# Kernel tuning notes

Measured on AMD Instinct MI355X. Metric: run time of the kernel, lower is better.

## Reference

```python
import jax, jax.numpy as jnp
import numpy as np

DIM = 128
NUM_HEADS = 4
WIN = 16  # effective window: window_size(8) * sqrt(dim_t=4)
N = WIN * WIN
B_ = 512
NW = 64


def _relative_position_index(wh, ww):
    coords = np.stack(np.meshgrid(np.arange(wh), np.arange(ww), indexing='ij'))  # (2,wh,ww)
    cf = coords.reshape(2, -1)
    rel = cf[:, :, None] - cf[:, None, :]  # (2,N,N)
    rel = rel.transpose(1, 2, 0).copy()
    rel[:, :, 0] += wh - 1
    rel[:, :, 1] += ww - 1
    rel[:, :, 0] *= 2 * ww - 1
    return rel.sum(-1).astype(np.int32)  # (N,N)


def setup_inputs() -> dict:
    key = jax.random.key(0)
    ks = jax.random.split(key, 7)
    inputs = jax.random.normal(ks[0], (B_, N, DIM), dtype=jnp.float32)
    mask = jax.random.normal(ks[1], (NW, N, N), dtype=jnp.float32)
    qkv_w = jax.random.normal(ks[2], (3 * DIM, DIM), dtype=jnp.float32) * 0.02
    qkv_b = jnp.zeros((3 * DIM,), dtype=jnp.float32)
    proj_w = jax.random.normal(ks[3], (DIM, DIM), dtype=jnp.float32) * 0.02
    proj_b = jnp.zeros((DIM,), dtype=jnp.float32)
    table_sz = (2 * WIN - 1) * (2 * WIN - 1)  # 961
    bias_table = jax.random.normal(ks[4], (table_sz, NUM_HEADS), dtype=jnp.float32) * 0.02
    rel_idx = jnp.asarray(_relative_position_index(WIN, WIN))  # (N,N) int32
    return {"inputs": inputs, "mask": mask, "qkv_w": qkv_w, "qkv_b": qkv_b,
            "proj_w": proj_w, "proj_b": proj_b, "bias_table": bias_table,
            "rel_idx": rel_idx}


def reference(inputs, mask, qkv_w, qkv_b, proj_w, proj_b, bias_table, rel_idx):
    B, Nn, C = inputs.shape
    H = bias_table.shape[1]
    Dh = C // H
    scale = Dh ** -0.5
    qkv = (inputs @ qkv_w.T + qkv_b).reshape(B, Nn, 3, H, Dh)
    qkv = jnp.transpose(qkv, (2, 0, 3, 1, 4))  # (3,B,H,N,Dh)
    q, k, v = qkv[0] * scale, qkv[1], qkv[2]
    attn = jnp.einsum('bhnd,bhmd->bhnm', q, k)  # (B,H,N,N)
    rpb = jnp.transpose(bias_table[rel_idx], (2, 0, 1))  # (H,N,N)
    attn = attn + rpb[None]
    nW = mask.shape[0]
    attn = attn.reshape(B // nW, nW, H, Nn, Nn) + mask[None, :, None]
    attn = jax.nn.softmax(attn.reshape(B, H, Nn, Nn), axis=-1)
    out = jnp.einsum('bhnm,bhmd->bhnd', attn, v)
    out = jnp.transpose(out, (0, 2, 1, 3)).reshape(B, Nn, C)
    return out @ proj_w.T + proj_b
```

## Files before the change

### kernel.cpp

```cpp
#include <hip/hip_runtime.h>

typedef __bf16 bf16;
typedef __bf16 bf16x8 __attribute__((ext_vector_type(8)));
typedef __bf16 bf16x4 __attribute__((ext_vector_type(4)));
typedef float f32x4 __attribute__((ext_vector_type(4)));

static __device__ __forceinline__ f32x4 mfma16(bf16x8 a, bf16x8 b, f32x4 c) {
  return __builtin_amdgcn_mfma_f32_16x16x32_bf16(a, b, c, 0, 0, 0);
}

static __device__ __forceinline__ bf16x8 pk8(f32x4 a, f32x4 b) {
  bf16x8 r;
  r[0] = (bf16)a[0]; r[1] = (bf16)a[1]; r[2] = (bf16)a[2]; r[3] = (bf16)a[3];
  r[4] = (bf16)b[0]; r[5] = (bf16)b[1]; r[6] = (bf16)b[2]; r[7] = (bf16)b[3];
  return r;
}

__global__ void k0_rpb(const float* __restrict__ bt, const int* __restrict__ ri,
                       float* __restrict__ rpb) {
  int t = blockIdx.x * 256 + threadIdx.x;
  int idx = ri[t];
  f32x4 v = *(const f32x4*)(bt + idx * 4);
#pragma unroll
  for (int h = 0; h < 4; ++h) rpb[h * 65536 + t] = v[h];
}

__global__ void k0_w(const float* __restrict__ qw, const float* __restrict__ pw,
                     bf16* __restrict__ wqb, bf16* __restrict__ wpb) {
  int t = blockIdx.x * 256 + threadIdx.x;
  if (t < 49152) wqb[t] = (bf16)qw[t];
  else wpb[t - 49152] = (bf16)pw[t - 49152];
}

__global__ void __launch_bounds__(256, 3)
k1_qkv(const float* __restrict__ x, const bf16* __restrict__ wqb,
       const float* __restrict__ qb, bf16* __restrict__ q_s,
       bf16* __restrict__ k_s, bf16* __restrict__ vt) {
  __shared__ bf16 xsm[16384];
  const int tid = threadIdx.x;
  const int wv = tid >> 6, ln = tid & 15, qd = (tid >> 4) & 3;
  const int b = blockIdx.x >> 1, half = blockIdx.x & 1;
  const int rg = wv >> 1, cg = wv & 1;

#pragma unroll
  for (int j = 0; j < 8; ++j) {
    const int bidx = j * 256 + tid;
    const int row = bidx >> 4, c = bidx & 15;
    const float* g = x + (size_t)(b * 256 + half * 128 + row) * 128 + c * 8;
    f32x4 a = *(const f32x4*)g, b2 = *(const f32x4*)(g + 4);
    *(bf16x8*)(xsm + row * 128 + ((c ^ (row & 7)) * 8)) = pk8(a, b2);
  }
  __syncthreads();

  f32x4 acc[4][4];
  bf16x8 xfk[4];

#pragma unroll
  for (int ch = 0; ch < 2; ++ch) {
#pragma unroll
    for (int mt = 0; mt < 4; ++mt)
#pragma unroll
      for (int nt = 0; nt < 4; ++nt) acc[mt][nt] = (f32x4){0.f, 0.f, 0.f, 0.f};
#pragma unroll
    for (int ks = 0; ks < 4; ++ks) {
#pragma unroll
      for (int nt = 0; nt < 4; ++nt) {
        const int row_l = rg * 64 + nt * 16 + ln;
        xfk[nt] = *(const bf16x8*)(xsm + row_l * 128 + (((ks * 4 + qd) ^ (ln & 7)) * 8));
      }
#pragma unroll
      for (int mt = 0; mt < 4; ++mt) {
        bf16x8 wf = *(const bf16x8*)(wqb + (size_t)(ch * 128 + cg * 64 + mt * 16 + ln) * 128 +
                                     ks * 32 + qd * 8);
#pragma unroll
        for (int nt = 0; nt < 4; ++nt) acc[mt][nt] = mfma16(wf, xfk[nt], acc[mt][nt]);
      }
    }
    const float scl = ch ? 1.0f : 0.17677669529663689f;
#pragma unroll
    for (int mt = 0; mt < 4; ++mt) {
      const int c0 = cg * 64 + mt * 16 + qd * 4;
      f32x4 b4 = *(const f32x4*)(qb + ch * 128 + c0);
      const int hh = c0 >> 5, d0 = c0 & 31;
#pragma unroll
      for (int nt = 0; nt < 4; ++nt) {
        const int nr = half * 128 + rg * 64 + nt * 16 + ln;
        bf16x4 o;
#pragma unroll
        for (int r = 0; r < 4; ++r) o[r] = (bf16)((acc[mt][nt][r] + b4[r]) * scl);
        const size_t base = (size_t)(b * 4 + hh) * 8192;
        if (ch == 0) {
          *(bf16x4*)(q_s + base + nr * 32 + d0) = o;
        } else {
          const int cb = (d0 >> 3) ^ (nr & 3) ^ ((nr >> 2) & 3);
          *(bf16x4*)(k_s + base + nr * 32 + cb * 8 + (d0 & 7)) = o;
        }
      }
    }
  }

#pragma unroll
  for (int nt = 0; nt < 4; ++nt)
#pragma unroll
    for (int mt = 0; mt < 4; ++mt) acc[nt][mt] = (f32x4){0.f, 0.f, 0.f, 0.f};
#pragma unroll
  for (int ks = 0; ks < 4; ++ks) {
#pragma unroll
    for (int nt = 0; nt < 4; ++nt) {
      const int row_l = rg * 64 + nt * 16 + ln;
      xfk[nt] = *(const bf16x8*)(xsm + row_l * 128 + (((ks * 4 + qd) ^ (ln & 7)) * 8));
    }
#pragma unroll
    for (int mt = 0; mt < 4; ++mt) {
      bf16x8 wf = *(const bf16x8*)(wqb + (size_t)(256 + cg * 64 + mt * 16 + ln) * 128 +
                                   ks * 32 + qd * 8);
#pragma unroll
      for (int nt = 0; nt < 4; ++nt) acc[nt][mt] = mfma16(xfk[nt], wf, acc[nt][mt]);
    }
  }
#pragma unroll
  for (int nt = 0; nt < 4; ++nt)
#pragma unroll
    for (int mt = 0; mt < 4; ++mt) {
      const int c = cg * 64 + mt * 16 + ln;
      const float bb = qb[256 + c];
      const int hh = c >> 5, dd = c & 31;
      const int n0 = half * 128 + rg * 64 + nt * 16 + qd * 4;
      bf16x4 o;
#pragma unroll
      for (int r = 0; r < 4; ++r) o[r] = (bf16)(acc[nt][mt][r] + bb);
      const int p = (n0 >> 3) ^ (dd & 7);
      *(bf16x4*)(vt + (size_t)(b * 4 + hh) * 8192 + dd * 256 + p * 8 + (n0 & 7)) = o;
    }
}

__global__ void __launch_bounds__(256, 3)
k2_attn(const bf16* __restrict__ q_s, const bf16* __restrict__ k_s,
        const bf16* __restrict__ vt, const float* __restrict__ mask,
        const float* __restrict__ rpb, float* __restrict__ ao) {
  __shared__ bf16 ksm[8192];
  __shared__ bf16 vsm[8192];
  __shared__ bf16 psm[8192];
  const int tid = threadIdx.x, wv = tid >> 6;
  const int ln = tid & 15, qd = (tid >> 4) & 3;
  const int w = blockIdx.x & 63, h = (blockIdx.x >> 6) & 3, rh = blockIdx.x >> 8;
  const int s = rh * 4 + wv;
  const int swzk = qd ^ (ln & 3) ^ ((ln >> 2) & 3);

  bf16x4 cmb[16];
  {
    const int n = s * 16 + ln;
#pragma unroll
    for (int mt = 0; mt < 16; ++mt) {
      f32x4 m4 = *(const f32x4*)(mask + ((size_t)w * 256 + n) * 256 + mt * 16 + qd * 4);
      f32x4 r4 = *(const f32x4*)(rpb + (size_t)h * 65536 + n * 256 + mt * 16 + qd * 4);
      bf16x4 cv;
#pragma unroll
      for (int r = 0; r < 4; ++r) cv[r] = (bf16)(m4[r] + r4[r]);
      cmb[mt] = cv;
    }
  }

  bf16x8 kr[4], vr[4];
  {
    const size_t base = (size_t)(w * 4 + h) * 8192;
#pragma unroll
    for (int i = 0; i < 4; ++i) {
      kr[i] = *(const bf16x8*)(k_s + base + i * 2048 + tid * 8);
      vr[i] = *(const bf16x8*)(vt + base + i * 2048 + tid * 8);
    }
  }

  for (int ib = 0; ib < 8; ++ib) {
    const int b = w + ib * 64;
    __syncthreads();
#pragma unroll
    for (int i = 0; i < 4; ++i) {
      *(bf16x8*)(ksm + i * 2048 + tid * 8) = kr[i];
      *(bf16x8*)(vsm + i * 2048 + tid * 8) = vr[i];
    }
    __syncthreads();
    if (ib < 7) {
      const size_t base = (size_t)((w + (ib + 1) * 64) * 4 + h) * 8192;
#pragma unroll
      for (int i = 0; i < 4; ++i) {
        kr[i] = *(const bf16x8*)(k_s + base + i * 2048 + tid * 8);
        vr[i] = *(const bf16x8*)(vt + base + i * 2048 + tid * 8);
      }
    }

    bf16x8 qf = *(const bf16x8*)(q_s + (size_t)(b * 4 + h) * 8192 + (s * 16 + ln) * 32 + qd * 8);
    float sum = 0.f;
    f32x4 accO[2];
    accO[0] = (f32x4){0.f, 0.f, 0.f, 0.f};
    accO[1] = (f32x4){0.f, 0.f, 0.f, 0.f};
    bf16* pb = psm + wv * 2048 + ln * 128;

#pragma unroll
    for (int hk = 0; hk < 2; ++hk) {
      f32x4 acc[8];
#pragma unroll
      for (int i = 0; i < 8; ++i) acc[i] = (f32x4){0.f, 0.f, 0.f, 0.f};
#pragma unroll
      for (int i = 0; i < 8; ++i) {
        const int m = (hk * 8 + i) * 16 + ln;
        bf16x8 af = *(const bf16x8*)(ksm + m * 32 + swzk * 8);
        acc[i] = mfma16(af, qf, acc[i]);
      }
#pragma unroll
      for (int i = 0; i < 8; ++i) {
        const int mt = hk * 8 + i;
        bf16x4 pv;
#pragma unroll
        for (int r = 0; r < 4; ++r) {
          float p = __expf(acc[i][r] + (float)cmb[mt][r]);
          sum += p;
          pv[r] = (bf16)p;
        }
        const int p16 = (i * 2 + (qd >> 1)) ^ (ln & 7);
        *(bf16x4*)(pb + p16 * 8 + (qd & 1) * 4) = pv;
      }
#pragma unroll
      for (int kt = 0; kt < 4; ++kt) {
        bf16x8 pf = *(const bf16x8*)(pb + (((kt * 4 + qd) ^ (ln & 7)) * 8));
#pragma unroll
        for (int ct = 0; ct < 2; ++ct) {
          const int d = ct * 16 + ln;
          const int p32 = ((hk * 4 + kt) * 4 + qd) ^ (d & 7);
          bf16x8 vf = *(const bf16x8*)(vsm + d * 256 + p32 * 8);
          accO[ct] = mfma16(pf, vf, accO[ct]);
        }
      }
    }
    sum += __shfl_xor(sum, 16);
    sum += __shfl_xor(sum, 32);
    const float linv = 1.0f / sum;
#pragma unroll
    for (int r = 0; r < 4; ++r) {
      const float lb = __shfl(linv, qd * 4 + r);
      const size_t orow = (size_t)(b * 256 + s * 16 + qd * 4 + r) * 128 + h * 32;
#pragma unroll
      for (int ct = 0; ct < 2; ++ct) ao[orow + ct * 16 + ln] = accO[ct][r] * lb;
    }
  }
}

__global__ void __launch_bounds__(256, 3)
k3_proj(const float* __restrict__ xin, const bf16* __restrict__ wpb,
        const float* __restrict__ pbias, float* __restrict__ out) {
  __shared__ bf16 xsm[16384];
  const int tid = threadIdx.x;
  const int wv = tid >> 6, ln = tid & 15, qd = (tid >> 4) & 3;
  const int rg = wv >> 1, cg = wv & 1;
  const size_t row0 = (size_t)blockIdx.x * 128;

#pragma unroll
  for (int j = 0; j < 8; ++j) {
    const int bidx = j * 256 + tid;
    const int row = bidx >> 4, c = bidx & 15;
    const float* g = xin + (row0 + row) * 128 + c * 8;
    f32x4 a = *(const f32x4*)g, b2 = *(const f32x4*)(g + 4);
    *(bf16x8*)(xsm + row * 128 + ((c ^ (row & 7)) * 8)) = pk8(a, b2);
  }
  __syncthreads();

  f32x4 acc[4][4];
  bf16x8 xfk[4];
#pragma unroll
  for (int mt = 0; mt < 4; ++mt)
#pragma unroll
    for (int nt = 0; nt < 4; ++nt) acc[mt][nt] = (f32x4){0.f, 0.f, 0.f, 0.f};
#pragma unroll
  for (int ks = 0; ks < 4; ++ks) {
#pragma unroll
    for (int nt = 0; nt < 4; ++nt) {
      const int row_l = rg * 64 + nt * 16 + ln;
      xfk[nt] = *(const bf16x8*)(xsm + row_l * 128 + (((ks * 4 + qd) ^ (ln & 7)) * 8));
    }
#pragma unroll
    for (int mt = 0; mt < 4; ++mt) {
      bf16x8 wf = *(const bf16x8*)(wpb + (size_t)(cg * 64 + mt * 16 + ln) * 128 +
                                   ks * 32 + qd * 8);
#pragma unroll
      for (int nt = 0; nt < 4; ++nt) acc[mt][nt] = mfma16(wf, xfk[nt], acc[mt][nt]);
    }
  }
#pragma unroll
  for (int mt = 0; mt < 4; ++mt) {
    const int c0 = cg * 64 + mt * 16 + qd * 4;
    f32x4 b4 = *(const f32x4*)(pbias + c0);
#pragma unroll
    for (int nt = 0; nt < 4; ++nt) {
      f32x4 o;
#pragma unroll
      for (int r = 0; r < 4; ++r) o[r] = acc[mt][nt][r] + b4[r];
      *(f32x4*)(out + (row0 + rg * 64 + nt * 16 + ln) * 128 + c0) = o;
    }
  }
}

extern "C" void kernel_launch(void* const* d_in, const int* in_sizes, int n_in,
                              void* d_out, int out_size, void* d_ws, size_t ws_size,
                              hipStream_t stream) {
  const float* x = (const float*)d_in[0];
  const float* mask = (const float*)d_in[1];
  const float* qkv_w = (const float*)d_in[2];
  const float* qkv_b = (const float*)d_in[3];
  const float* proj_w = (const float*)d_in[4];
  const float* proj_b = (const float*)d_in[5];
  const float* bias_table = (const float*)d_in[6];
  const int* rel_idx = (const int*)d_in[7];

  char* ws = (char*)d_ws;
  bf16* q_s = (bf16*)ws;
  bf16* k_s = (bf16*)(ws + 33554432ll);
  bf16* vt = (bf16*)(ws + 67108864ll);
  float* rpb = (float*)(ws + 100663296ll);
  bf16* wqb = (bf16*)(ws + 101711872ll);
  bf16* wpb = wqb + 49152;
  float* ao = (float*)d_out;

  k0_rpb<<<dim3(256), dim3(256), 0, stream>>>(bias_table, rel_idx, rpb);
  k0_w<<<dim3(256), dim3(256), 0, stream>>>(qkv_w, proj_w, wqb, wpb);
  k1_qkv<<<dim3(1024), dim3(256), 0, stream>>>(x, wqb, qkv_b, q_s, k_s, vt);
  k2_attn<<<dim3(1024), dim3(256), 0, stream>>>(q_s, k_s, vt, mask, rpb, ao);
  k3_proj<<<dim3(1024), dim3(256), 0, stream>>>(ao, wpb, proj_b, (float*)d_out);
}
```

Measured before the change: 311.5 us.

## Restructure attention to one wave per head, keep K/V in registers

```diff
diff --git a/kernel.cpp b/kernel.cpp
--- a/kernel.cpp
+++ b/kernel.cpp
@@ -16,20 +16,28 @@
   return r;
 }
 
-__global__ void k0_rpb(const float* __restrict__ bt, const int* __restrict__ ri,
-                       float* __restrict__ rpb) {
-  int t = blockIdx.x * 256 + threadIdx.x;
-  int idx = ri[t];
-  f32x4 v = *(const f32x4*)(bt + idx * 4);
-#pragma unroll
-  for (int h = 0; h < 4; ++h) rpb[h * 65536 + t] = v[h];
-}
-
-__global__ void k0_w(const float* __restrict__ qw, const float* __restrict__ pw,
-                     bf16* __restrict__ wqb, bf16* __restrict__ wpb) {
-  int t = blockIdx.x * 256 + threadIdx.x;
-  if (t < 49152) wqb[t] = (bf16)qw[t];
-  else wpb[t - 49152] = (bf16)pw[t - 49152];
+__global__ void k0_prep(const float* __restrict__ qw, const float* __restrict__ pw,
+                        const float* __restrict__ bt, const int* __restrict__ ri,
+                        const float* __restrict__ mask, bf16* __restrict__ wqb,
+                        bf16* __restrict__ wpb, bf16* __restrict__ rpb_bf,
+                        bf16* __restrict__ mask_bf) {
+  const int bid = blockIdx.x, tid = threadIdx.x;
+  if (bid < 256) {
+    int t = bid * 256 + tid;
+    if (t < 49152) wqb[t] = (bf16)qw[t];
+    else wpb[t - 49152] = (bf16)pw[t - 49152];
+  } else if (bid < 512) {
+    int t = (bid - 256) * 256 + tid;
+    int idx = ri[t];
+    f32x4 v = *(const f32x4*)(bt + idx * 4);
+#pragma unroll
+    for (int h = 0; h < 4; ++h) rpb_bf[h * 65536 + t] = (bf16)v[h];
+  } else {
+    int i = (bid - 512) * 256 + tid;
+    f32x4 a = *(const f32x4*)(mask + (size_t)i * 8);
+    f32x4 b = *(const f32x4*)(mask + (size_t)i * 8 + 4);
+    *(bf16x8*)(mask_bf + (size_t)i * 8) = pk8(a, b);
+  }
 }
 
 __global__ void __launch_bounds__(256, 3)
@@ -77,6 +85,7 @@
       }
     }
     const float scl = ch ? 1.0f : 0.17677669529663689f;
+    bf16* dst = ch ? k_s : q_s;
 #pragma unroll
     for (int mt = 0; mt < 4; ++mt) {
       const int c0 = cg * 64 + mt * 16 + qd * 4;
@@ -88,13 +97,7 @@
         bf16x4 o;
 #pragma unroll
         for (int r = 0; r < 4; ++r) o[r] = (bf16)((acc[mt][nt][r] + b4[r]) * scl);
-        const size_t base = (size_t)(b * 4 + hh) * 8192;
-        if (ch == 0) {
-          *(bf16x4*)(q_s + base + nr * 32 + d0) = o;
-        } else {
-          const int cb = (d0 >> 3) ^ (nr & 3) ^ ((nr >> 2) & 3);
-          *(bf16x4*)(k_s + base + nr * 32 + cb * 8 + (d0 & 7)) = o;
-        }
+        *(bf16x4*)(dst + (size_t)(b * 4 + hh) * 8192 + nr * 32 + d0) = o;
       }
     }
   }
@@ -129,91 +132,63 @@
       bf16x4 o;
 #pragma unroll
       for (int r = 0; r < 4; ++r) o[r] = (bf16)(acc[nt][mt][r] + bb);
-      const int p = (n0 >> 3) ^ (dd & 7);
-      *(bf16x4*)(vt + (size_t)(b * 4 + hh) * 8192 + dd * 256 + p * 8 + (n0 & 7)) = o;
-    }
-}
-
-__global__ void __launch_bounds__(256, 3)
+      *(bf16x4*)(vt + (size_t)(b * 4 + hh) * 8192 + dd * 256 + n0) = o;
+    }
+}
+
+__global__ void __launch_bounds__(64, 2)
 k2_attn(const bf16* __restrict__ q_s, const bf16* __restrict__ k_s,
-        const bf16* __restrict__ vt, const float* __restrict__ mask,
-        const float* __restrict__ rpb, float* __restrict__ ao) {
-  __shared__ bf16 ksm[8192];
-  __shared__ bf16 vsm[8192];
-  __shared__ bf16 psm[8192];
-  const int tid = threadIdx.x, wv = tid >> 6;
-  const int ln = tid & 15, qd = (tid >> 4) & 3;
-  const int w = blockIdx.x & 63, h = (blockIdx.x >> 6) & 3, rh = blockIdx.x >> 8;
-  const int s = rh * 4 + wv;
-  const int swzk = qd ^ (ln & 3) ^ ((ln >> 2) & 3);
-
-  bf16x4 cmb[16];
-  {
-    const int n = s * 16 + ln;
-#pragma unroll
-    for (int mt = 0; mt < 16; ++mt) {
-      f32x4 m4 = *(const f32x4*)(mask + ((size_t)w * 256 + n) * 256 + mt * 16 + qd * 4);
-      f32x4 r4 = *(const f32x4*)(rpb + (size_t)h * 65536 + n * 256 + mt * 16 + qd * 4);
-      bf16x4 cv;
-#pragma unroll
-      for (int r = 0; r < 4; ++r) cv[r] = (bf16)(m4[r] + r4[r]);
-      cmb[mt] = cv;
-    }
-  }
-
-  bf16x8 kr[4], vr[4];
-  {
-    const size_t base = (size_t)(w * 4 + h) * 8192;
-#pragma unroll
-    for (int i = 0; i < 4; ++i) {
-      kr[i] = *(const bf16x8*)(k_s + base + i * 2048 + tid * 8);
-      vr[i] = *(const bf16x8*)(vt + base + i * 2048 + tid * 8);
-    }
-  }
-
-  for (int ib = 0; ib < 8; ++ib) {
-    const int b = w + ib * 64;
-    __syncthreads();
-#pragma unroll
-    for (int i = 0; i < 4; ++i) {
-      *(bf16x8*)(ksm + i * 2048 + tid * 8) = kr[i];
-      *(bf16x8*)(vsm + i * 2048 + tid * 8) = vr[i];
-    }
-    __syncthreads();
-    if (ib < 7) {
-      const size_t base = (size_t)((w + (ib + 1) * 64) * 4 + h) * 8192;
-#pragma unroll
-      for (int i = 0; i < 4; ++i) {
-        kr[i] = *(const bf16x8*)(k_s + base + i * 2048 + tid * 8);
-        vr[i] = *(const bf16x8*)(vt + base + i * 2048 + tid * 8);
-      }
-    }
-
-    bf16x8 qf = *(const bf16x8*)(q_s + (size_t)(b * 4 + h) * 8192 + (s * 16 + ln) * 32 + qd * 8);
+        const bf16* __restrict__ vt, const bf16* __restrict__ mask_bf,
+        const bf16* __restrict__ rpb_bf, float* __restrict__ ao) {
+  __shared__ bf16 psm[2048];
+  const int tid = threadIdx.x, ln = tid & 15, qd = tid >> 4;
+  const int h = blockIdx.x & 3, b = blockIdx.x >> 2, w = b & 63;
+
+  const size_t panel = (size_t)(b * 4 + h) * 8192;
+  bf16x8 kf[16], vf[16];
+#pragma unroll
+  for (int mt = 0; mt < 16; ++mt)
+    kf[mt] = *(const bf16x8*)(k_s + panel + (mt * 16 + ln) * 32 + qd * 8);
+#pragma unroll
+  for (int k8 = 0; k8 < 8; ++k8)
+#pragma unroll
+    for (int ct = 0; ct < 2; ++ct)
+      vf[k8 * 2 + ct] = *(const bf16x8*)(vt + panel + (ct * 16 + ln) * 256 + k8 * 32 + qd * 8);
+
+  const bf16* mrow = mask_bf + (size_t)w * 65536;
+  const bf16* rrow = rpb_bf + (size_t)h * 65536;
+  const bf16* qp = q_s + panel;
+  bf16* pb = psm + ln * 128;
+
+  for (int s = 0; s < 16; ++s) {
+    bf16x8 qf = *(const bf16x8*)(qp + (s * 16 + ln) * 32 + qd * 8);
+    const int nrow = s * 16 + ln;
     float sum = 0.f;
     f32x4 accO[2];
     accO[0] = (f32x4){0.f, 0.f, 0.f, 0.f};
     accO[1] = (f32x4){0.f, 0.f, 0.f, 0.f};
-    bf16* pb = psm + wv * 2048 + ln * 128;
 
 #pragma unroll
     for (int hk = 0; hk < 2; ++hk) {
+      bf16x4 mm[8], rr[8];
+#pragma unroll
+      for (int i = 0; i < 8; ++i) {
+        const int off = nrow * 256 + (hk * 8 + i) * 16 + qd * 4;
+        mm[i] = *(const bf16x4*)(mrow + off);
+        rr[i] = *(const bf16x4*)(rrow + off);
+      }
       f32x4 acc[8];
 #pragma unroll
       for (int i = 0; i < 8; ++i) acc[i] = (f32x4){0.f, 0.f, 0.f, 0.f};
 #pragma unroll
+      for (int i = 0; i < 8; ++i)
+        acc[i] = mfma16(kf[hk * 8 + i], qf, acc[i]);
+#pragma unroll
       for (int i = 0; i < 8; ++i) {
-        const int m = (hk * 8 + i) * 16 + ln;
-        bf16x8 af = *(const bf16x8*)(ksm + m * 32 + swzk * 8);
-        acc[i] = mfma16(af, qf, acc[i]);
-      }
-#pragma unroll
-      for (int i = 0; i < 8; ++i) {
-        const int mt = hk * 8 + i;
         bf16x4 pv;
 #pragma unroll
         for (int r = 0; r < 4; ++r) {
-          float p = __expf(acc[i][r] + (float)cmb[mt][r]);
+          float p = __expf(acc[i][r] + (float)mm[i][r] + (float)rr[i][r]);
           sum += p;
           pv[r] = (bf16)p;
         }
@@ -224,12 +199,8 @@
       for (int kt = 0; kt < 4; ++kt) {
         bf16x8 pf = *(const bf16x8*)(pb + (((kt * 4 + qd) ^ (ln & 7)) * 8));
 #pragma unroll
-        for (int ct = 0; ct < 2; ++ct) {
-          const int d = ct * 16 + ln;
-          const int p32 = ((hk * 4 + kt) * 4 + qd) ^ (d & 7);
-          bf16x8 vf = *(const bf16x8*)(vsm + d * 256 + p32 * 8);
-          accO[ct] = mfma16(pf, vf, accO[ct]);
-        }
+        for (int ct = 0; ct < 2; ++ct)
+          accO[ct] = mfma16(pf, vf[(hk * 4 + kt) * 2 + ct], accO[ct]);
       }
     }
     sum += __shfl_xor(sum, 16);
@@ -315,14 +286,15 @@
   bf16* q_s = (bf16*)ws;
   bf16* k_s = (bf16*)(ws + 33554432ll);
   bf16* vt = (bf16*)(ws + 67108864ll);
-  float* rpb = (float*)(ws + 100663296ll);
-  bf16* wqb = (bf16*)(ws + 101711872ll);
+  bf16* mask_bf = (bf16*)(ws + 100663296ll);
+  bf16* rpb_bf = (bf16*)(ws + 109051904ll);
+  bf16* wqb = (bf16*)(ws + 109576192ll);
   bf16* wpb = wqb + 49152;
   float* ao = (float*)d_out;
 
-  k0_rpb<<<dim3(256), dim3(256), 0, stream>>>(bias_table, rel_idx, rpb);
-  k0_w<<<dim3(256), dim3(256), 0, stream>>>(qkv_w, proj_w, wqb, wpb);
+  k0_prep<<<dim3(2560), dim3(256), 0, stream>>>(qkv_w, proj_w, bias_table, rel_idx,
+                                                mask, wqb, wpb, rpb_bf, mask_bf);
   k1_qkv<<<dim3(1024), dim3(256), 0, stream>>>(x, wqb, qkv_b, q_s, k_s, vt);
-  k2_attn<<<dim3(1024), dim3(256), 0, stream>>>(q_s, k_s, vt, mask, rpb, ao);
+  k2_attn<<<dim3(2048), dim3(64), 0, stream>>>(q_s, k_s, vt, mask_bf, rpb_bf, ao);
   k3_proj<<<dim3(1024), dim3(256), 0, stream>>>(ao, wpb, proj_b, (float*)d_out);
 }
```

Result: slower. 337.4 us (+8.3%).
